# Performance work log

Measured on AMD Instinct MI355X. Metric: run time of the kernel, lower is better.

The kernel has to match this reference:

```python
import jax, jax.numpy as jnp
import numpy as np

D_K = 64


def setup_inputs() -> dict:
    key = jax.random.key(0)
    ks = jax.random.split(key, 12)
    b, n, t, k = 16, 2048, 12, 32
    d_q, d_k, d_c, n_head, d_out = 32, 64, 10, 4, 32
    return {
        "x": jax.random.normal(ks[0], (b, n, t, k), dtype=jnp.float32),
        "dis_mat": jax.random.uniform(ks[1], (n, n), dtype=jnp.float32),
        "K_S": jax.random.normal(ks[2], (n_head, d_k), dtype=jnp.float32) * 0.1,
        "V_S": jax.random.normal(ks[3], (n_head, n, d_c), dtype=jnp.float32) * 0.05,
        "K_T": jax.random.normal(ks[4], (n_head, d_k), dtype=jnp.float32) * 0.1,
        "V_T": jax.random.normal(ks[5], (n_head, n, d_c), dtype=jnp.float32) * 0.05,
        "W_Q0": jax.random.normal(ks[6], (k, d_q), dtype=jnp.float32) * 0.1,
        "W_QS": jax.random.normal(ks[7], (n * d_q, d_k), dtype=jnp.float32) * 0.01,
        "W_QT": jax.random.normal(ks[8], (t * d_q, d_k), dtype=jnp.float32) * 0.05,
        "W2": jax.random.normal(ks[9], (k, d_out), dtype=jnp.float32) * 0.1,
        "W_s0": jax.random.normal(ks[10], (k, d_out), dtype=jnp.float32) * 0.1,
        "W_s1": jax.random.normal(ks[11], (k, d_out), dtype=jnp.float32) * 0.1,
    }


def reference(x, dis_mat, K_S, V_S, K_T, V_T, W_Q0, W_QS, W_QT, W2, W_s0, W_s1):
    b, n, t, k = x.shape
    scale = 1.0 / jnp.sqrt(jnp.float32(D_K))
    # Q_0 projection: [b,n,t,d_q]
    out = x @ W_Q0
    # temporal / spatial queries -> [b, d_k]
    qt = out.mean(axis=1).reshape(b, -1) @ W_QT
    qs = out.mean(axis=2).reshape(b, -1) @ W_QS
    # head attention weights: [b, n_head]
    attn_t = jax.nn.softmax((qt * scale) @ K_T.T, axis=1)
    attn_s = jax.nn.softmax((qs * scale) @ K_S.T, axis=1)
    # head-mixed node embeddings: [b, n, d_c]
    et = jnp.einsum('hnc,bh->bnc', V_T, attn_t)
    es = jnp.einsum('hnc,bh->bnc', V_S, attn_s)
    ets = et + es
    # dynamic adjacency: [b, n, n]
    adj = jnp.einsum('bnc,bmc->bnm', ets, ets)
    adj = jax.nn.softmax(jax.nn.relu(dis_mat[None] + adj), axis=2)
    # graph conv chain over [b, t, n, d_out]
    xp = jnp.transpose(x, (0, 2, 1, 3))  # [b,t,n,k]
    z = xp @ W2
    for W in (W_s0, W_s1):
        z = jnp.einsum('bnm,btmd->btnd', adj, z) + xp @ W
    return jnp.transpose(z, (0, 2, 1, 3))  # [b,n,t,d_out]
```

## Files before the change

kernel.cpp:

```cpp
#include <hip/hip_runtime.h>

typedef __bf16 bf16x8 __attribute__((ext_vector_type(8)));
typedef float f32x4 __attribute__((ext_vector_type(4)));

__device__ __forceinline__ unsigned short f2bf(float f) {
  unsigned u = __builtin_bit_cast(unsigned, f);
  u += 0x7fffu + ((u >> 16) & 1u);
  return (unsigned short)(u >> 16);
}
__device__ __forceinline__ float bf2f(unsigned short h) {
  unsigned u = ((unsigned)h) << 16;
  return __builtin_bit_cast(float, u);
}
__device__ __forceinline__ unsigned char f2fp8(float v) {
  return (unsigned char)(__builtin_amdgcn_cvt_pk_fp8_f32(v, v, 0, false) & 0xff);
}
__device__ __forceinline__ void gload16(const void* g, void* l) {
  __builtin_amdgcn_global_load_lds((const __attribute__((address_space(1))) void*)g,
                                   (__attribute__((address_space(3))) void*)l, 16, 0, 0);
}
__device__ __forceinline__ int perm7(int x) {
  return ((x >> 3) & 3) * 32 + ((x >> 5) << 3) + (x & 7);
}


__global__ __launch_bounds__(256) void k_xmn(const float* __restrict__ x,
                                             float* __restrict__ pxmn) {
  int bx = blockIdx.x;
  int b = bx / 48, r = bx % 48, t = r >> 2, c = r & 3;
  int k = threadIdx.x & 31, sl = threadIdx.x >> 5;
  const float* xp = x + (size_t)b * 786432 + (size_t)(c * 512) * 384 + (size_t)t * 32 + k;
  float s = 0.f;
  for (int i = 0; i < 64; ++i) s += xp[(size_t)((sl << 6) + i) * 384];
  __shared__ float red[8][32];
  red[sl][k] = s;
  __syncthreads();
  if (threadIdx.x < 32) {
    float tot = 0.f;
#pragma unroll
    for (int j = 0; j < 8; ++j) tot += red[j][threadIdx.x];
    pxmn[((c * 16 + b) * 12 + t) * 32 + threadIdx.x] = tot;
  }
}

__global__ __launch_bounds__(256) void k_qs(const float* __restrict__ x,
                                            const float* __restrict__ W_Q0,
                                            const float* __restrict__ W_QS,
                                            float* __restrict__ pqs) {
  __shared__ __align__(16) float w0[1024];
  __shared__ __align__(16) float lm[1024];
  __shared__ float lq[1024];
  __shared__ float red[4][16][64];
  const int tid = threadIdx.x;
#pragma unroll
  for (int i = 0; i < 4; ++i) w0[tid + i * 256] = W_Q0[tid + i * 256];
  const int n0 = blockIdx.x * 2;

  {
    const int b = tid >> 4, r = tid & 15, n = r >> 3, k4 = r & 7;
    const float4* xp = (const float4*)(x + ((size_t)(b * 2048 + n0 + n) * 12) * 32) + k4;
    float4 s0 = xp[0], s1 = xp[8], s2 = xp[16];
    float4 s3 = xp[24], s4 = xp[32], s5 = xp[40];
#pragma unroll
    for (int t = 6; t < 12; ++t) {
      float4 v = xp[t * 8];
      s0.x += v.x; s0.y += v.y; s0.z += v.z; s0.w += v.w;
      float4 tmp = s0; s0 = s1; s1 = s2; s2 = s3; s3 = s4; s4 = s5; s5 = tmp;
    }
    float4 m;
    m.x = (s0.x + s1.x + s2.x) + (s3.x + s4.x + s5.x);
    m.y = (s0.y + s1.y + s2.y) + (s3.y + s4.y + s5.y);
    m.z = (s0.z + s1.z + s2.z) + (s3.z + s4.z + s5.z);
    m.w = (s0.w + s1.w + s2.w) + (s3.w + s4.w + s5.w);
    const float inv12 = 1.0f / 12.0f;
    m.x *= inv12; m.y *= inv12; m.z *= inv12; m.w *= inv12;
    *(float4*)(lm + (b * 2 + n) * 32 + k4 * 4) = m;
  }
  __syncthreads();
#pragma unroll
  for (int j = 0; j < 4; ++j) {
    int i = tid + j * 256;
    int bn = i >> 5, q = i & 31;
    const float* mrow = &lm[bn * 32];
    float a = 0.f;
#pragma unroll
    for (int k = 0; k < 32; ++k) a += mrow[k] * w0[k * 32 + q];
    lq[i] = a;
  }
  __syncthreads();
  const int lane = tid & 63, w = tid >> 6;
  float acc[16];
#pragma unroll
  for (int b = 0; b < 16; ++b) acc[b] = 0.f;
#pragma unroll
  for (int rl = 0; rl < 16; ++rl) {
    int r = w * 16 + rl;
    float wv = W_QS[(size_t)(n0 * 32 + r) * 64 + lane];
#pragma unroll
    for (int b = 0; b < 16; ++b) acc[b] += lq[b * 64 + r] * wv;
  }
#pragma unroll
  for (int b = 0; b < 16; ++b) red[w][b][lane] = acc[b];
  __syncthreads();
#pragma unroll
  for (int it = 0; it < 4; ++it) {
    int idx = tid + it * 256;
    float s = red[0][idx >> 6][idx & 63] + red[1][idx >> 6][idx & 63] +
              red[2][idx >> 6][idx & 63] + red[3][idx >> 6][idx & 63];
    pqs[(size_t)blockIdx.x * 1024 + idx] = s;
  }
}

__global__ __launch_bounds__(256) void k_head(const float* __restrict__ pqs,
                                              const float* __restrict__ pxmn,
                                              const float* __restrict__ W_Q0,
                                              const float* __restrict__ W_QT,
                                              const float* __restrict__ K_T,
                                              const float* __restrict__ K_S,
                                              float* __restrict__ at_g) {
  const int b = blockIdx.x, tid = threadIdx.x;
  __shared__ float red[4][64];
  __shared__ float qs_s[64];
  __shared__ float xmn_s[384];
  __shared__ float xp[384];
  __shared__ float qtp[4][64];

  {
    const int q = tid >> 6, dk = tid & 63;
    const float* p = pqs + (size_t)(q * 256) * 1024 + b * 64 + dk;
    float s0 = 0.f, s1 = 0.f, s2 = 0.f, s3 = 0.f;
#pragma unroll
    for (int c = 0; c < 256; c += 4) {
      s0 += p[(size_t)(c + 0) * 1024];
      s1 += p[(size_t)(c + 1) * 1024];
      s2 += p[(size_t)(c + 2) * 1024];
      s3 += p[(size_t)(c + 3) * 1024];
    }
    red[q][dk] = (s0 + s1) + (s2 + s3);
  }
  for (int i = tid; i < 384; i += 256) {
    float v = pxmn[(b * 12) * 32 + i] + pxmn[((16 + b) * 12) * 32 + i] +
              pxmn[((32 + b) * 12) * 32 + i] + pxmn[((48 + b) * 12) * 32 + i];
    xmn_s[i] = v * (1.0f / 2048.0f);
  }
  __syncthreads();
  for (int i = tid; i < 384; i += 256) {
    int t = i >> 5, q = i & 31;
    float a = 0.f;
#pragma unroll
    for (int k = 0; k < 32; ++k) a += xmn_s[t * 32 + k] * W_Q0[k * 32 + q];
    xp[i] = a;
  }
  if (tid < 64) qs_s[tid] = red[0][tid] + red[1][tid] + red[2][tid] + red[3][tid];
  __syncthreads();
  {
    const int w = tid >> 6, dk = tid & 63;
    const float* wq = W_QT + (size_t)(w * 96) * 64 + dk;
    const float* xw = xp + w * 96;
    float a0 = 0.f, a1 = 0.f, a2 = 0.f;
#pragma unroll
    for (int i = 0; i < 96; i += 3) {
      a0 += xw[i + 0] * wq[(size_t)(i + 0) * 64];
      a1 += xw[i + 1] * wq[(size_t)(i + 1) * 64];
      a2 += xw[i + 2] * wq[(size_t)(i + 2) * 64];
    }
    qtp[w][dk] = (a0 + a1) + a2;
  }
  __syncthreads();
  if (tid < 64) {
    int lane = tid;
    float qtv = qtp[0][lane] + qtp[1][lane] + qtp[2][lane] + qtp[3][lane];
    float qsv = qs_s[lane];
    float lt[4], ls[4];
#pragma unroll
    for (int h = 0; h < 4; ++h) {
      float p = qtv * K_T[h * 64 + lane];
#pragma unroll
      for (int off = 32; off > 0; off >>= 1) p += __shfl_xor(p, off);
      lt[h] = p;
      float p2 = qsv * K_S[h * 64 + lane];
#pragma unroll
      for (int off = 32; off > 0; off >>= 1) p2 += __shfl_xor(p2, off);
      ls[h] = p2;
    }
    if (lane == 0) {
      const float scale = 0.125f;
      float mt = fmaxf(fmaxf(lt[0], lt[1]), fmaxf(lt[2], lt[3]));
      float ms = fmaxf(fmaxf(ls[0], ls[1]), fmaxf(ls[2], ls[3]));
      float et[4], es[4], st = 0.f, ss = 0.f;
#pragma unroll
      for (int h = 0; h < 4; ++h) {
        et[h] = __expf((lt[h] - mt) * scale); st += et[h];
        es[h] = __expf((ls[h] - ms) * scale); ss += es[h];
      }
#pragma unroll
      for (int h = 0; h < 4; ++h) {
        at_g[b * 8 + h] = et[h] / st;
        at_g[b * 8 + 4 + h] = es[h] / ss;
      }
    }
  }
}

__global__ __launch_bounds__(256) void k_ets(const float* __restrict__ at_g,
                                             const float* __restrict__ V_T,
                                             const float* __restrict__ V_S,
                                             unsigned short* __restrict__ ets_bf) {
  int idx = blockIdx.x * 256 + threadIdx.x;
  int b = idx >> 11, n = idx & 2047;
  const float* at = at_g + b * 8;
  float a0 = at[0], a1 = at[1], a2 = at[2], a3 = at[3];
  float s0 = at[4], s1 = at[5], s2 = at[6], s3 = at[7];
  float v[10];
#pragma unroll
  for (int c = 0; c < 10; ++c) {
    int o = n * 10 + c;
    v[c] = a0 * V_T[o] + a1 * V_T[20480 + o] + a2 * V_T[40960 + o] + a3 * V_T[61440 + o] +
           s0 * V_S[o] + s1 * V_S[20480 + o] + s2 * V_S[40960 + o] + s3 * V_S[61440 + o];
  }
  uint4 lo, hi;
  lo.x = (unsigned)f2bf(v[0]) | ((unsigned)f2bf(v[1]) << 16);
  lo.y = (unsigned)f2bf(v[2]) | ((unsigned)f2bf(v[3]) << 16);
  lo.z = (unsigned)f2bf(v[4]) | ((unsigned)f2bf(v[5]) << 16);
  lo.w = (unsigned)f2bf(v[6]) | ((unsigned)f2bf(v[7]) << 16);
  hi.x = (unsigned)f2bf(v[8]) | ((unsigned)f2bf(v[9]) << 16);
  hi.y = 0; hi.z = 0; hi.w = 0;
  *(uint4*)(ets_bf + (size_t)idx * 16) = lo;
  *(uint4*)(ets_bf + (size_t)idx * 16 + 8) = hi;
}


__global__ __launch_bounds__(512, 4) void k_adj(const unsigned short* __restrict__ ets_bf,
                                                const float* __restrict__ dis,
                                                unsigned char* __restrict__ adjf) {
  __shared__ __align__(16) unsigned char Bsh[65536];
  __shared__ float st_max[8][16];
  __shared__ float st_sum[8][16];
  __shared__ float rowmax_s[16];
  __shared__ float rowinv_s[16];

  const int tid = threadIdx.x;
  const int lane = tid & 63;
  const int w = tid >> 6;
  const int cl = lane & 15;
  const int g = lane >> 4;
  const int b = blockIdx.x >> 7;
  const int n0 = (blockIdx.x & 127) << 4;

  const unsigned char* gsrc = (const unsigned char*)(ets_bf + (size_t)b * 32768);
#pragma unroll
  for (int it = 0; it < 8; ++it)
    gload16(gsrc + it * 8192 + tid * 16, Bsh + it * 8192 + (w << 10));
  __syncthreads();

  uint4 araw = *(const uint4*)(ets_bf + ((size_t)b * 2048 + n0 + cl) * 16 + (g & 1) * 8);
  if (g >= 2) { araw.x = 0; araw.y = 0; araw.z = 0; araw.w = 0; }
  bf16x8 afrag = __builtin_bit_cast(bf16x8, araw);

  f32x4 acc[16];
  const int cbase = (w << 8) + cl;
#pragma unroll
  for (int n = 0; n < 16; ++n) {
    uint4 braw = *(const uint4*)(Bsh + (size_t)(cbase + n * 16) * 32 + (g & 1) * 16);
    if (g >= 2) { braw.x = 0; braw.y = 0; braw.z = 0; braw.w = 0; }
    bf16x8 bfrag = __builtin_bit_cast(bf16x8, braw);
    acc[n] = __builtin_amdgcn_mfma_f32_16x16x32_bf16(afrag, bfrag, (f32x4){0.f, 0.f, 0.f, 0.f},
                                                     0, 0, 0);
  }

  float mx[4] = {-1e30f, -1e30f, -1e30f, -1e30f};
  const float* dbase = dis + (size_t)(n0 + g * 4) * 2048 + (w << 8) + cl;
#pragma unroll
  for (int n = 0; n < 16; ++n) {
#pragma unroll
    for (int j = 0; j < 4; ++j) {
      float s = fmaxf(acc[n][j] + dbase[(size_t)j * 2048 + n * 16], 0.f);
      acc[n][j] = s;
      mx[j] = fmaxf(mx[j], s);
    }
  }
#pragma unroll
  for (int j = 0; j < 4; ++j) {
    mx[j] = fmaxf(mx[j], __shfl_xor(mx[j], 1));
    mx[j] = fmaxf(mx[j], __shfl_xor(mx[j], 2));
    mx[j] = fmaxf(mx[j], __shfl_xor(mx[j], 4));
    mx[j] = fmaxf(mx[j], __shfl_xor(mx[j], 8));
  }
  if (cl == 0) {
#pragma unroll
    for (int j = 0; j < 4; ++j) st_max[w][g * 4 + j] = mx[j];
  }
  __syncthreads();
  if (tid < 16) {
    float m = st_max[0][tid];
#pragma unroll
    for (int ww = 1; ww < 8; ++ww) m = fmaxf(m, st_max[ww][tid]);
    rowmax_s[tid] = m;
  }
  __syncthreads();

  float rm[4], sm[4] = {0.f, 0.f, 0.f, 0.f};
#pragma unroll
  for (int j = 0; j < 4; ++j) rm[j] = rowmax_s[g * 4 + j];
#pragma unroll
  for (int n = 0; n < 16; ++n) {
#pragma unroll
    for (int j = 0; j < 4; ++j) {
      float e = __expf(acc[n][j] - rm[j]);
      acc[n][j] = e;
      sm[j] += e;
    }
  }
#pragma unroll
  for (int j = 0; j < 4; ++j) {
    sm[j] += __shfl_xor(sm[j], 1);
    sm[j] += __shfl_xor(sm[j], 2);
    sm[j] += __shfl_xor(sm[j], 4);
    sm[j] += __shfl_xor(sm[j], 8);
  }
  if (cl == 0) {
#pragma unroll
    for (int j = 0; j < 4; ++j) st_sum[w][g * 4 + j] = sm[j];
  }
  __syncthreads();
  if (tid < 16) {
    float s = st_sum[0][tid];
#pragma unroll
    for (int ww = 1; ww < 8; ++ww) s += st_sum[ww][tid];
    rowinv_s[tid] = 256.0f / s;
  }
  __syncthreads();

  unsigned char* Tw = Bsh + (w << 12);
  float inv[4];
#pragma unroll
  for (int j = 0; j < 4; ++j) inv[j] = rowinv_s[g * 4 + j];
#pragma unroll
  for (int n = 0; n < 16; ++n) {
    int ml = n * 16 + cl;
    int pb = ((ml >> 7) << 7) + perm7(ml & 127);
#pragma unroll
    for (int j = 0; j < 4; ++j)
      Tw[(g * 4 + j) * 256 + pb] = f2fp8(acc[n][j] * inv[j]);
  }
  __syncthreads();

  unsigned char* obase = adjf + ((size_t)b * 2048 + n0) * 2048 + (w << 8);
#pragma unroll
  for (int r = 0; r < 16; ++r) {
    unsigned v = *(const unsigned*)(Tw + r * 256 + lane * 4);
    *(unsigned*)(obase + (size_t)r * 2048 + lane * 4) = v;
  }
}


__global__ __launch_bounds__(256) void k_zb(const float* __restrict__ x,
                                            const float* __restrict__ W2,
                                            const float* __restrict__ Ws0,
                                            const float* __restrict__ Ws1,
                                            unsigned char* __restrict__ z0Tf,
                                            unsigned short* __restrict__ bias0T,
                                            unsigned short* __restrict__ bias1T) {
  __shared__ __align__(16) unsigned short wlds[3072];
  const int tid = threadIdx.x;
  for (int j = tid; j < 3072; j += 256) {
    int mat = j >> 10, r = j & 1023, k = r >> 5, d = r & 31;
    const float* Wsrc = (mat == 0) ? W2 : (mat == 1 ? Ws0 : Ws1);
    wlds[(mat * 32 + d) * 32 + k] = f2bf(Wsrc[r]);
  }
  __syncthreads();

  const int lane = tid & 63, w = tid >> 6;
  const int cl = lane & 15, g = lane >> 4;
  const int bx = blockIdx.x;
  const int b = bx / 48, r = bx % 48, t = r >> 2, mc = r & 3;
  const int m0w = mc * 512 + w * 128;

  bf16x8 bfr[6];
#pragma unroll
  for (int dt = 0; dt < 6; ++dt)
    bfr[dt] = *(const bf16x8*)(wlds + (dt * 16 + cl) * 32 + g * 8);

  const float* gx = x + ((size_t)(b * 2048 + m0w + cl) * 12 + t) * 32 + g * 8;
  unsigned char* z0base = z0Tf + (size_t)b * 786432 + (size_t)(t * 32) * 2048;
  unsigned short* b0base = bias0T + (size_t)b * 786432 + (size_t)(t * 32) * 2048;
  unsigned short* b1base = bias1T + (size_t)b * 786432 + (size_t)(t * 32) * 2048;

#pragma unroll
  for (int i = 0; i < 8; ++i) {
    const float* xp = gx + (size_t)i * 16 * 384;
    float4 v0 = *(const float4*)xp;
    float4 v1 = *(const float4*)(xp + 4);
    bf16x8 af;
    af[0] = (__bf16)v0.x; af[1] = (__bf16)v0.y; af[2] = (__bf16)v0.z; af[3] = (__bf16)v0.w;
    af[4] = (__bf16)v1.x; af[5] = (__bf16)v1.y; af[6] = (__bf16)v1.z; af[7] = (__bf16)v1.w;
    f32x4 acc[6];
#pragma unroll
    for (int dt = 0; dt < 6; ++dt)
      acc[dt] = __builtin_amdgcn_mfma_f32_16x16x32_bf16(af, bfr[dt],
                                                        (f32x4){0.f, 0.f, 0.f, 0.f}, 0, 0, 0);
    const int m = m0w + i * 16 + g * 4;
    const int pb = ((m >> 7) << 7) + perm7(m & 127);
#pragma unroll
    for (int dt = 0; dt < 2; ++dt) {
      unsigned u = __builtin_amdgcn_cvt_pk_fp8_f32(acc[dt][0], acc[dt][1], 0, false);
      u = __builtin_amdgcn_cvt_pk_fp8_f32(acc[dt][2], acc[dt][3], (int)u, true);
      *(unsigned*)(z0base + (size_t)(dt * 16 + cl) * 2048 + pb) = u;
    }
#pragma unroll
    for (int dt = 0; dt < 2; ++dt) {
      uint2 p;
      p.x = (unsigned)f2bf(acc[2 + dt][0]) | ((unsigned)f2bf(acc[2 + dt][1]) << 16);
      p.y = (unsigned)f2bf(acc[2 + dt][2]) | ((unsigned)f2bf(acc[2 + dt][3]) << 16);
      *(uint2*)(b0base + (size_t)(dt * 16 + cl) * 2048 + m) = p;
      uint2 q;
      q.x = (unsigned)f2bf(acc[4 + dt][0]) | ((unsigned)f2bf(acc[4 + dt][1]) << 16);
      q.y = (unsigned)f2bf(acc[4 + dt][2]) | ((unsigned)f2bf(acc[4 + dt][3]) << 16);
      *(uint2*)(b1base + (size_t)(dt * 16 + cl) * 2048 + m) = q;
    }
  }
}


template <int OUT_F32>
__global__ __launch_bounds__(256, 2) void gemm_adj(const unsigned char* __restrict__ adjf,
                                                   const unsigned char* __restrict__ Bt,
                                                   const unsigned short* __restrict__ biasT,
                                                   void* __restrict__ outp) {
  const int tid = threadIdx.x;
  const int lane = tid & 63;
  const int wid = tid >> 6;
  const int wr = wid >> 1, wc = wid & 1;
  const int orig = blockIdx.x;
  const int wg = (orig & 7) * 64 + (orig >> 3);
  const int b = wg >> 5;
  const int w32 = wg & 31;
  const int m0 = ((w32 >> 1) & 15) << 7;
  const int c0 = (w32 & 1) * 192;

  __shared__ __align__(16) unsigned char smem[81920];

  const unsigned char* aBase = adjf + ((size_t)b << 22);
  const unsigned char* bBase = Bt + (size_t)b * 786432;
  const int jx = ((tid & 7) ^ ((tid >> 3) & 7)) << 4;
  const unsigned char* gA = aBase + (size_t)(m0 + (tid >> 3)) * 2048 + jx;
  const unsigned char* gB = bBase + (size_t)(c0 + (tid >> 3)) * 2048 + jx;

  int aoff[2][4], boff[2][6];
#pragma unroll
  for (int kkp = 0; kkp < 2; ++kkp) {
    int c = ((lane >> 4) << 1) + kkp;
#pragma unroll
    for (int f = 0; f < 4; ++f) {
      int rA = wr * 64 + f * 16 + (lane & 15);
      aoff[kkp][f] = rA * 128 + ((c ^ (rA & 7)) << 4);
    }
#pragma unroll
    for (int n = 0; n < 6; ++n) {
      int rB = wc * 96 + n * 16 + (lane & 15);
      boff[kkp][n] = 16384 + rB * 128 + ((c ^ (rB & 7)) << 4);
    }
  }

  f32x4 acc[4][6] = {};

#define STAGE(BUF, KT)                                                               \
  {                                                                                  \
    _Pragma("unroll") for (int ii = 0; ii < 4; ++ii)                                 \
        gload16(gA + (size_t)ii * 65536 + (KT)*128, smem + (BUF) + ii * 4096 + tid * 16); \
    _Pragma("unroll") for (int ii = 0; ii < 6; ++ii)                                 \
        gload16(gB + (size_t)ii * 65536 + (KT)*128,                                  \
                smem + (BUF) + 16384 + ii * 4096 + tid * 16);                        \
  }

  STAGE(0, 0);

  int cur = 0;
  for (int kt = 0; kt < 16; ++kt) {
    const int nxt = cur ^ 40960;
    if (kt < 15) {
      STAGE(nxt, kt + 1);
      asm volatile("s_waitcnt vmcnt(10)" ::: "memory");
    } else {
      asm volatile("s_waitcnt vmcnt(0)" ::: "memory");
    }
    __builtin_amdgcn_s_barrier();
#pragma unroll
    for (int kkp = 0; kkp < 2; ++kkp) {
      ulong2 av[4], bv[6];
#pragma unroll
      for (int f = 0; f < 4; ++f) av[f] = *(const ulong2*)(smem + cur + aoff[kkp][f]);
#pragma unroll
      for (int n = 0; n < 6; ++n) bv[n] = *(const ulong2*)(smem + cur + boff[kkp][n]);
#pragma unroll
      for (int m = 0; m < 4; ++m)
#pragma unroll
        for (int n = 0; n < 6; ++n)
          acc[m][n] = __builtin_amdgcn_mfma_f32_16x16x32_fp8_fp8(
              (long)av[m].x, (long)bv[n].x, acc[m][n], 0, 0, 0);
#pragma unroll
      for (int m = 0; m < 4; ++m)
#pragma unroll
        for (int n = 0; n < 6; ++n)
          acc[m][n] = __builtin_amdgcn_mfma_f32_16x16x32_fp8_fp8(
              (long)av[m].y, (long)bv[n].y, acc[m][n], 0, 0, 0);
    }
    __builtin_amdgcn_s_barrier();
    cur = nxt;
  }
#undef STAGE

  const float inv256 = 0.00390625f;
  const int cl = lane & 15;
  const int r4 = (lane >> 4) << 2;
  const unsigned short* bi = biasT + (size_t)b * 786432;
  if (OUT_F32) {
    float* o = (float*)outp + (size_t)b * 786432;
#pragma unroll
    for (int m = 0; m < 4; ++m) {
      int row0 = m0 + wr * 64 + m * 16 + r4;
#pragma unroll
      for (int n = 0; n < 6; ++n) {
        int col = c0 + wc * 96 + n * 16 + cl;
        uint2 bw = *(const uint2*)(bi + ((size_t)col << 11) + row0);
        float bv0 = bf2f((unsigned short)(bw.x & 0xffff));
        float bv1 = bf2f((unsigned short)(bw.x >> 16));
        float bv2 = bf2f((unsigned short)(bw.y & 0xffff));
        float bv3 = bf2f((unsigned short)(bw.y >> 16));
        o[(size_t)(row0 + 0) * 384 + col] = acc[m][n][0] * inv256 + bv0;
        o[(size_t)(row0 + 1) * 384 + col] = acc[m][n][1] * inv256 + bv1;
        o[(size_t)(row0 + 2) * 384 + col] = acc[m][n][2] * inv256 + bv2;
        o[(size_t)(row0 + 3) * 384 + col] = acc[m][n][3] * inv256 + bv3;
      }
    }
  } else {
    unsigned char* o = (unsigned char*)outp + (size_t)b * 786432;
#pragma unroll
    for (int m = 0; m < 4; ++m) {
      int row0 = m0 + wr * 64 + m * 16 + r4;
      const int pb = ((row0 >> 7) << 7) + perm7(row0 & 127);
#pragma unroll
      for (int n = 0; n < 6; ++n) {
        int col = c0 + wc * 96 + n * 16 + cl;
        uint2 bw = *(const uint2*)(bi + ((size_t)col << 11) + row0);
        float v0 = acc[m][n][0] * inv256 + bf2f((unsigned short)(bw.x & 0xffff));
        float v1 = acc[m][n][1] * inv256 + bf2f((unsigned short)(bw.x >> 16));
        float v2 = acc[m][n][2] * inv256 + bf2f((unsigned short)(bw.y & 0xffff));
        float v3 = acc[m][n][3] * inv256 + bf2f((unsigned short)(bw.y >> 16));
        unsigned u = __builtin_amdgcn_cvt_pk_fp8_f32(v0, v1, 0, false);
        u = __builtin_amdgcn_cvt_pk_fp8_f32(v2, v3, (int)u, true);
        *(unsigned*)(o + (size_t)col * 2048 + pb) = u;
      }
    }
  }
}


extern "C" void kernel_launch(void* const* d_in, const int* in_sizes, int n_in,
                              void* d_out, int out_size, void* d_ws, size_t ws_size,
                              hipStream_t stream) {
  const float* x = (const float*)d_in[0];
  const float* dis = (const float*)d_in[1];
  const float* K_S = (const float*)d_in[2];
  const float* V_S = (const float*)d_in[3];
  const float* K_T = (const float*)d_in[4];
  const float* V_T = (const float*)d_in[5];
  const float* W_Q0 = (const float*)d_in[6];
  const float* W_QS = (const float*)d_in[7];
  const float* W_QT = (const float*)d_in[8];
  const float* W2 = (const float*)d_in[9];
  const float* W_s0 = (const float*)d_in[10];
  const float* W_s1 = (const float*)d_in[11];

  char* ws = (char*)d_ws;
  float* pxmn = (float*)(ws + 0);
  float* pqs = (float*)(ws + 98304);
  unsigned short* ets_bf = (unsigned short*)(ws + 4292608);
  unsigned char* adjf = (unsigned char*)(ws + 5341184);
  unsigned char* z0Tf = (unsigned char*)(ws + 72450048);
  unsigned char* z1Tf = (unsigned char*)(ws + 85032960);
  unsigned short* bias0T = (unsigned short*)(ws + 97615872);
  unsigned short* bias1T = (unsigned short*)(ws + 122781696);
  float* at_g = (float*)(ws + 147947520);

  k_xmn<<<768, 256, 0, stream>>>(x, pxmn);
  k_qs<<<1024, 256, 0, stream>>>(x, W_Q0, W_QS, pqs);
  k_head<<<16, 256, 0, stream>>>(pqs, pxmn, W_Q0, W_QT, K_T, K_S, at_g);
  k_ets<<<128, 256, 0, stream>>>(at_g, V_T, V_S, ets_bf);
  k_adj<<<2048, 512, 0, stream>>>(ets_bf, dis, adjf);
  k_zb<<<768, 256, 0, stream>>>(x, W2, W_s0, W_s1, z0Tf, bias0T, bias1T);
  gemm_adj<0><<<512, 256, 0, stream>>>(adjf, z0Tf, bias0T, (void*)z1Tf);
  gemm_adj<1><<<512, 256, 0, stream>>>(adjf, z1Tf, bias1T, d_out);
}
```

Measured before the change: 197.6 us.

## Fuse node-mean into k_zb, drop softmax max pass, stage stores in LDS

Removes the separate k_xmn kernel. Its sum of x over nodes is now computed inside k_zb from the x values that kernel already loads, and written as per-chunk partials that k_head adds up. That saves one full read of x. k_adj swaps the MFMA operands so each lane owns an adjacency row, reads dis with float4 loads, and drops the row-max pass and its barriers. This relies on relu keeping the exponent non-negative and small enough not to overflow. k_zb and k_adj now stage outputs in padded LDS so global writes are coalesced 16-byte stores, and k_zb runs twice as many blocks.

```diff
diff --git a/kernel.cpp b/kernel.cpp
--- a/kernel.cpp
+++ b/kernel.cpp
@@ -12,9 +12,6 @@
   unsigned u = ((unsigned)h) << 16;
   return __builtin_bit_cast(float, u);
 }
-__device__ __forceinline__ unsigned char f2fp8(float v) {
-  return (unsigned char)(__builtin_amdgcn_cvt_pk_fp8_f32(v, v, 0, false) & 0xff);
-}
 __device__ __forceinline__ void gload16(const void* g, void* l) {
   __builtin_amdgcn_global_load_lds((const __attribute__((address_space(1))) void*)g,
                                    (__attribute__((address_space(3))) void*)l, 16, 0, 0);
@@ -23,25 +20,6 @@
   return ((x >> 3) & 3) * 32 + ((x >> 5) << 3) + (x & 7);
 }
 
-
-__global__ __launch_bounds__(256) void k_xmn(const float* __restrict__ x,
-                                             float* __restrict__ pxmn) {
-  int bx = blockIdx.x;
-  int b = bx / 48, r = bx % 48, t = r >> 2, c = r & 3;
-  int k = threadIdx.x & 31, sl = threadIdx.x >> 5;
-  const float* xp = x + (size_t)b * 786432 + (size_t)(c * 512) * 384 + (size_t)t * 32 + k;
-  float s = 0.f;
-  for (int i = 0; i < 64; ++i) s += xp[(size_t)((sl << 6) + i) * 384];
-  __shared__ float red[8][32];
-  red[sl][k] = s;
-  __syncthreads();
-  if (threadIdx.x < 32) {
-    float tot = 0.f;
-#pragma unroll
-    for (int j = 0; j < 8; ++j) tot += red[j][threadIdx.x];
-    pxmn[((c * 16 + b) * 12 + t) * 32 + threadIdx.x] = tot;
-  }
-}
 
 __global__ __launch_bounds__(256) void k_qs(const float* __restrict__ x,
                                             const float* __restrict__ W_Q0,
@@ -112,7 +90,7 @@
 }
 
 __global__ __launch_bounds__(256) void k_head(const float* __restrict__ pqs,
-                                              const float* __restrict__ pxmn,
+                                              const float* __restrict__ pxmn_p,
                                               const float* __restrict__ W_Q0,
                                               const float* __restrict__ W_QT,
                                               const float* __restrict__ K_T,
@@ -139,8 +117,9 @@
     red[q][dk] = (s0 + s1) + (s2 + s3);
   }
   for (int i = tid; i < 384; i += 256) {
-    float v = pxmn[(b * 12) * 32 + i] + pxmn[((16 + b) * 12) * 32 + i] +
-              pxmn[((32 + b) * 12) * 32 + i] + pxmn[((48 + b) * 12) * 32 + i];
+    int t = i >> 5, k = i & 31;
+    const float* p = pxmn_p + (size_t)((b * 12 + t) * 8) * 32 + k;
+    float v = ((p[0] + p[32]) + (p[64] + p[96])) + ((p[128] + p[160]) + (p[192] + p[224]));
     xmn_s[i] = v * (1.0f / 2048.0f);
   }
   __syncthreads();
@@ -234,9 +213,7 @@
                                                 const float* __restrict__ dis,
                                                 unsigned char* __restrict__ adjf) {
   __shared__ __align__(16) unsigned char Bsh[65536];
-  __shared__ float st_max[8][16];
   __shared__ float st_sum[8][16];
-  __shared__ float rowmax_s[16];
   __shared__ float rowinv_s[16];
 
   const int tid = threadIdx.x;
@@ -255,7 +232,7 @@
 
   uint4 araw = *(const uint4*)(ets_bf + ((size_t)b * 2048 + n0 + cl) * 16 + (g & 1) * 8);
   if (g >= 2) { araw.x = 0; araw.y = 0; araw.z = 0; araw.w = 0; }
-  bf16x8 afrag = __builtin_bit_cast(bf16x8, araw);
+  bf16x8 strip = __builtin_bit_cast(bf16x8, araw);
 
   f32x4 acc[16];
   const int cbase = (w << 8) + cl;
@@ -263,65 +240,26 @@
   for (int n = 0; n < 16; ++n) {
     uint4 braw = *(const uint4*)(Bsh + (size_t)(cbase + n * 16) * 32 + (g & 1) * 16);
     if (g >= 2) { braw.x = 0; braw.y = 0; braw.z = 0; braw.w = 0; }
-    bf16x8 bfrag = __builtin_bit_cast(bf16x8, braw);
-    acc[n] = __builtin_amdgcn_mfma_f32_16x16x32_bf16(afrag, bfrag, (f32x4){0.f, 0.f, 0.f, 0.f},
-                                                     0, 0, 0);
-  }
-
-  float mx[4] = {-1e30f, -1e30f, -1e30f, -1e30f};
-  const float* dbase = dis + (size_t)(n0 + g * 4) * 2048 + (w << 8) + cl;
+    bf16x8 nodes = __builtin_bit_cast(bf16x8, braw);
+    acc[n] = __builtin_amdgcn_mfma_f32_16x16x32_bf16(nodes, strip,
+                                                     (f32x4){0.f, 0.f, 0.f, 0.f}, 0, 0, 0);
+  }
+
+  const float* drow = dis + (size_t)(n0 + cl) * 2048 + (w << 8) + (g << 2);
+  float lsum = 0.f;
 #pragma unroll
   for (int n = 0; n < 16; ++n) {
-#pragma unroll
-    for (int j = 0; j < 4; ++j) {
-      float s = fmaxf(acc[n][j] + dbase[(size_t)j * 2048 + n * 16], 0.f);
-      acc[n][j] = s;
-      mx[j] = fmaxf(mx[j], s);
-    }
-  }
-#pragma unroll
-  for (int j = 0; j < 4; ++j) {
-    mx[j] = fmaxf(mx[j], __shfl_xor(mx[j], 1));
-    mx[j] = fmaxf(mx[j], __shfl_xor(mx[j], 2));
-    mx[j] = fmaxf(mx[j], __shfl_xor(mx[j], 4));
-    mx[j] = fmaxf(mx[j], __shfl_xor(mx[j], 8));
-  }
-  if (cl == 0) {
-#pragma unroll
-    for (int j = 0; j < 4; ++j) st_max[w][g * 4 + j] = mx[j];
-  }
-  __syncthreads();
-  if (tid < 16) {
-    float m = st_max[0][tid];
-#pragma unroll
-    for (int ww = 1; ww < 8; ++ww) m = fmaxf(m, st_max[ww][tid]);
-    rowmax_s[tid] = m;
-  }
-  __syncthreads();
-
-  float rm[4], sm[4] = {0.f, 0.f, 0.f, 0.f};
-#pragma unroll
-  for (int j = 0; j < 4; ++j) rm[j] = rowmax_s[g * 4 + j];
-#pragma unroll
-  for (int n = 0; n < 16; ++n) {
-#pragma unroll
-    for (int j = 0; j < 4; ++j) {
-      float e = __expf(acc[n][j] - rm[j]);
-      acc[n][j] = e;
-      sm[j] += e;
-    }
-  }
-#pragma unroll
-  for (int j = 0; j < 4; ++j) {
-    sm[j] += __shfl_xor(sm[j], 1);
-    sm[j] += __shfl_xor(sm[j], 2);
-    sm[j] += __shfl_xor(sm[j], 4);
-    sm[j] += __shfl_xor(sm[j], 8);
-  }
-  if (cl == 0) {
-#pragma unroll
-    for (int j = 0; j < 4; ++j) st_sum[w][g * 4 + j] = sm[j];
-  }
+    float4 dv = *(const float4*)(drow + n * 16);
+    float e0 = __expf(fmaxf(acc[n][0] + dv.x, 0.f));
+    float e1 = __expf(fmaxf(acc[n][1] + dv.y, 0.f));
+    float e2 = __expf(fmaxf(acc[n][2] + dv.z, 0.f));
+    float e3 = __expf(fmaxf(acc[n][3] + dv.w, 0.f));
+    acc[n][0] = e0; acc[n][1] = e1; acc[n][2] = e2; acc[n][3] = e3;
+    lsum += (e0 + e1) + (e2 + e3);
+  }
+  lsum += __shfl_xor(lsum, 16);
+  lsum += __shfl_xor(lsum, 32);
+  if (g == 0) st_sum[w][cl] = lsum;
   __syncthreads();
   if (tid < 16) {
     float s = st_sum[0][tid];
@@ -331,25 +269,24 @@
   }
   __syncthreads();
 
-  unsigned char* Tw = Bsh + (w << 12);
-  float inv[4];
-#pragma unroll
-  for (int j = 0; j < 4; ++j) inv[j] = rowinv_s[g * 4 + j];
+  const float inv = rowinv_s[cl];
+  unsigned char* Tw = Bsh + w * 4352;
 #pragma unroll
   for (int n = 0; n < 16; ++n) {
-    int ml = n * 16 + cl;
+    int ml = n * 16 + (g << 2);
     int pb = ((ml >> 7) << 7) + perm7(ml & 127);
-#pragma unroll
-    for (int j = 0; j < 4; ++j)
-      Tw[(g * 4 + j) * 256 + pb] = f2fp8(acc[n][j] * inv[j]);
-  }
-  __syncthreads();
-
-  unsigned char* obase = adjf + ((size_t)b * 2048 + n0) * 2048 + (w << 8);
-#pragma unroll
-  for (int r = 0; r < 16; ++r) {
-    unsigned v = *(const unsigned*)(Tw + r * 256 + lane * 4);
-    *(unsigned*)(obase + (size_t)r * 2048 + lane * 4) = v;
+    unsigned u = __builtin_amdgcn_cvt_pk_fp8_f32(acc[n][0] * inv, acc[n][1] * inv, 0, false);
+    u = __builtin_amdgcn_cvt_pk_fp8_f32(acc[n][2] * inv, acc[n][3] * inv, (int)u, true);
+    *(unsigned*)(Tw + cl * 272 + pb) = u;
+  }
+  asm volatile("s_waitcnt lgkmcnt(0)" ::: "memory");
+
+  unsigned char* obase = adjf + ((size_t)(b * 2048 + n0)) * 2048 + (w << 8);
+  const int rr = lane >> 2, cc = (lane & 3) * 64;
+#pragma unroll
+  for (int q = 0; q < 4; ++q) {
+    uint4 v = *(const uint4*)(Tw + rr * 272 + cc + q * 16);
+    *(uint4*)(obase + (size_t)rr * 2048 + cc + q * 16) = v;
   }
 }
 
@@ -360,37 +297,41 @@
                                             const float* __restrict__ Ws1,
                                             unsigned char* __restrict__ z0Tf,
                                             unsigned short* __restrict__ bias0T,
-                                            unsigned short* __restrict__ bias1T) {
+                                            unsigned short* __restrict__ bias1T,
+                                            float* __restrict__ pxmn_p) {
   __shared__ __align__(16) unsigned short wlds[3072];
+  __shared__ __align__(16) unsigned char zsh[32 * 272];
+  __shared__ __align__(16) unsigned char b0sh[32 * 528];
+  __shared__ __align__(16) unsigned char b1sh[32 * 528];
+  __shared__ float psum[4][32];
   const int tid = threadIdx.x;
   for (int j = tid; j < 3072; j += 256) {
-    int mat = j >> 10, r = j & 1023, k = r >> 5, d = r & 31;
+    int mat = j >> 10, rr = j & 1023, k = rr >> 5, d = rr & 31;
     const float* Wsrc = (mat == 0) ? W2 : (mat == 1 ? Ws0 : Ws1);
-    wlds[(mat * 32 + d) * 32 + k] = f2bf(Wsrc[r]);
+    wlds[(mat * 32 + d) * 32 + k] = f2bf(Wsrc[rr]);
   }
   __syncthreads();
 
   const int lane = tid & 63, w = tid >> 6;
   const int cl = lane & 15, g = lane >> 4;
   const int bx = blockIdx.x;
-  const int b = bx / 48, r = bx % 48, t = r >> 2, mc = r & 3;
-  const int m0w = mc * 512 + w * 128;
+  const int b = bx / 96, r = bx % 96, t = r >> 3, mc = r & 7;
 
   bf16x8 bfr[6];
 #pragma unroll
   for (int dt = 0; dt < 6; ++dt)
     bfr[dt] = *(const bf16x8*)(wlds + (dt * 16 + cl) * 32 + g * 8);
 
-  const float* gx = x + ((size_t)(b * 2048 + m0w + cl) * 12 + t) * 32 + g * 8;
-  unsigned char* z0base = z0Tf + (size_t)b * 786432 + (size_t)(t * 32) * 2048;
-  unsigned short* b0base = bias0T + (size_t)b * 786432 + (size_t)(t * 32) * 2048;
-  unsigned short* b1base = bias1T + (size_t)b * 786432 + (size_t)(t * 32) * 2048;
-
-#pragma unroll
-  for (int i = 0; i < 8; ++i) {
+  const float* gx = x + ((size_t)(b * 2048 + mc * 256 + w * 64 + cl) * 12 + t) * 32 + g * 8;
+
+  float4 sx0 = {0.f, 0.f, 0.f, 0.f}, sx1 = {0.f, 0.f, 0.f, 0.f};
+#pragma unroll
+  for (int i = 0; i < 4; ++i) {
     const float* xp = gx + (size_t)i * 16 * 384;
     float4 v0 = *(const float4*)xp;
     float4 v1 = *(const float4*)(xp + 4);
+    sx0.x += v0.x; sx0.y += v0.y; sx0.z += v0.z; sx0.w += v0.w;
+    sx1.x += v1.x; sx1.y += v1.y; sx1.z += v1.z; sx1.w += v1.w;
     bf16x8 af;
     af[0] = (__bf16)v0.x; af[1] = (__bf16)v0.y; af[2] = (__bf16)v0.z; af[3] = (__bf16)v0.w;
     af[4] = (__bf16)v1.x; af[5] = (__bf16)v1.y; af[6] = (__bf16)v1.z; af[7] = (__bf16)v1.w;
@@ -399,24 +340,60 @@
     for (int dt = 0; dt < 6; ++dt)
       acc[dt] = __builtin_amdgcn_mfma_f32_16x16x32_bf16(af, bfr[dt],
                                                         (f32x4){0.f, 0.f, 0.f, 0.f}, 0, 0, 0);
-    const int m = m0w + i * 16 + g * 4;
-    const int pb = ((m >> 7) << 7) + perm7(m & 127);
+    const int ml = w * 64 + i * 16 + g * 4;
+    const int pb = ((ml >> 7) << 7) + perm7(ml & 127);
 #pragma unroll
     for (int dt = 0; dt < 2; ++dt) {
       unsigned u = __builtin_amdgcn_cvt_pk_fp8_f32(acc[dt][0], acc[dt][1], 0, false);
       u = __builtin_amdgcn_cvt_pk_fp8_f32(acc[dt][2], acc[dt][3], (int)u, true);
-      *(unsigned*)(z0base + (size_t)(dt * 16 + cl) * 2048 + pb) = u;
+      *(unsigned*)(zsh + (dt * 16 + cl) * 272 + pb) = u;
     }
 #pragma unroll
     for (int dt = 0; dt < 2; ++dt) {
       uint2 p;
       p.x = (unsigned)f2bf(acc[2 + dt][0]) | ((unsigned)f2bf(acc[2 + dt][1]) << 16);
       p.y = (unsigned)f2bf(acc[2 + dt][2]) | ((unsigned)f2bf(acc[2 + dt][3]) << 16);
-      *(uint2*)(b0base + (size_t)(dt * 16 + cl) * 2048 + m) = p;
+      *(uint2*)(b0sh + (dt * 16 + cl) * 528 + ml * 2) = p;
       uint2 q;
       q.x = (unsigned)f2bf(acc[4 + dt][0]) | ((unsigned)f2bf(acc[4 + dt][1]) << 16);
       q.y = (unsigned)f2bf(acc[4 + dt][2]) | ((unsigned)f2bf(acc[4 + dt][3]) << 16);
-      *(uint2*)(b1base + (size_t)(dt * 16 + cl) * 2048 + m) = q;
+      *(uint2*)(b1sh + (dt * 16 + cl) * 528 + ml * 2) = q;
+    }
+  }
+#pragma unroll
+  for (int off = 1; off < 16; off <<= 1) {
+    sx0.x += __shfl_xor(sx0.x, off); sx0.y += __shfl_xor(sx0.y, off);
+    sx0.z += __shfl_xor(sx0.z, off); sx0.w += __shfl_xor(sx0.w, off);
+    sx1.x += __shfl_xor(sx1.x, off); sx1.y += __shfl_xor(sx1.y, off);
+    sx1.z += __shfl_xor(sx1.z, off); sx1.w += __shfl_xor(sx1.w, off);
+  }
+  if (cl == 0) {
+    *(float4*)(&psum[w][g * 8]) = sx0;
+    *(float4*)(&psum[w][g * 8 + 4]) = sx1;
+  }
+  __syncthreads();
+  if (tid < 32)
+    pxmn_p[(size_t)((b * 12 + t) * 8 + mc) * 32 + tid] =
+        psum[0][tid] + psum[1][tid] + psum[2][tid] + psum[3][tid];
+
+  const int d = tid >> 3, c8 = tid & 7;
+  {
+    uint4 v0 = *(const uint4*)(zsh + d * 272 + c8 * 32);
+    uint4 v1 = *(const uint4*)(zsh + d * 272 + c8 * 32 + 16);
+    unsigned char* zdst =
+        z0Tf + (size_t)b * 786432 + (size_t)(t * 32 + d) * 2048 + mc * 256 + c8 * 32;
+    *(uint4*)zdst = v0;
+    *(uint4*)(zdst + 16) = v1;
+  }
+  {
+    char* bdst0 = (char*)(bias0T + (size_t)b * 786432 + (size_t)(t * 32 + d) * 2048 +
+                          mc * 256 + c8 * 32);
+    char* bdst1 = (char*)(bias1T + (size_t)b * 786432 + (size_t)(t * 32 + d) * 2048 +
+                          mc * 256 + c8 * 32);
+#pragma unroll
+    for (int q = 0; q < 4; ++q) {
+      *(uint4*)(bdst0 + q * 16) = *(const uint4*)(b0sh + d * 528 + c8 * 64 + q * 16);
+      *(uint4*)(bdst1 + q * 16) = *(const uint4*)(b1sh + d * 528 + c8 * 64 + q * 16);
     }
   }
 }
@@ -573,22 +550,21 @@
   const float* W_s1 = (const float*)d_in[11];
 
   char* ws = (char*)d_ws;
-  float* pxmn = (float*)(ws + 0);
-  float* pqs = (float*)(ws + 98304);
-  unsigned short* ets_bf = (unsigned short*)(ws + 4292608);
-  unsigned char* adjf = (unsigned char*)(ws + 5341184);
-  unsigned char* z0Tf = (unsigned char*)(ws + 72450048);
-  unsigned char* z1Tf = (unsigned char*)(ws + 85032960);
-  unsigned short* bias0T = (unsigned short*)(ws + 97615872);
-  unsigned short* bias1T = (unsigned short*)(ws + 122781696);
-  float* at_g = (float*)(ws + 147947520);
-
-  k_xmn<<<768, 256, 0, stream>>>(x, pxmn);
+  float* pxmn_p = (float*)(ws + 0);
+  float* pqs = (float*)(ws + 196608);
+  unsigned short* ets_bf = (unsigned short*)(ws + 4390912);
+  unsigned char* adjf = (unsigned char*)(ws + 5439488);
+  unsigned char* z0Tf = (unsigned char*)(ws + 72548352);
+  unsigned char* z1Tf = (unsigned char*)(ws + 85131264);
+  unsigned short* bias0T = (unsigned short*)(ws + 97714176);
+  unsigned short* bias1T = (unsigned short*)(ws + 122880000);
+  float* at_g = (float*)(ws + 148045824);
+
   k_qs<<<1024, 256, 0, stream>>>(x, W_Q0, W_QS, pqs);
-  k_head<<<16, 256, 0, stream>>>(pqs, pxmn, W_Q0, W_QT, K_T, K_S, at_g);
+  k_zb<<<1536, 256, 0, stream>>>(x, W2, W_s0, W_s1, z0Tf, bias0T, bias1T, pxmn_p);
+  k_head<<<16, 256, 0, stream>>>(pqs, pxmn_p, W_Q0, W_QT, K_T, K_S, at_g);
   k_ets<<<128, 256, 0, stream>>>(at_g, V_T, V_S, ets_bf);
   k_adj<<<2048, 512, 0, stream>>>(ets_bf, dis, adjf);
-  k_zb<<<768, 256, 0, stream>>>(x, W2, W_s0, W_s1, z0Tf, bias0T, bias1T);
   gemm_adj<0><<<512, 256, 0, stream>>>(adjf, z0Tf, bias0T, (void*)z1Tf);
   gemm_adj<1><<<512, 256, 0, stream>>>(adjf, z1Tf, bias1T, d_out);
 }
```

Result: no change. 200.9 us (+1.6%).
